# Performance work log

Measured on AMD Instinct MI355X. Metric: run time of the kernel, lower is better.

The kernel has to match this reference:

```python
import jax, jax.numpy as jnp
import numpy as np

B, S, D, A = 8, 4096, 128, 128


def _pos_encoding(seq_len, dim):
    # sin/cos positional encoding, same construction as the torch buffer
    pos = np.arange(seq_len, dtype=np.float32)[:, None]
    div = np.exp(np.arange(0, dim, 2, dtype=np.float32) * (-np.log(10000.0) / dim))
    pe = np.zeros((seq_len, dim), dtype=np.float32)
    pe[:, 0::2] = np.sin(pos * div)
    pe[:, 1::2] = np.cos(pos * div)
    return jnp.asarray(pe)


def setup_inputs() -> dict:
    key = jax.random.key(0)
    ks = jax.random.split(key, 7)
    sc = 1.0 / np.sqrt(D)
    return {
        "x": jax.random.normal(ks[0], (B, S, D), dtype=jnp.float32),
        "Wq": jax.random.normal(ks[1], (D, A), dtype=jnp.float32) * sc,
        "bq": jnp.zeros((A,), dtype=jnp.float32),
        "Wk": jax.random.normal(ks[2], (D, A), dtype=jnp.float32) * sc,
        "bk": jnp.zeros((A,), dtype=jnp.float32),
        "Wv": jax.random.normal(ks[3], (D, A), dtype=jnp.float32) * sc,
        "bv": jnp.zeros((A,), dtype=jnp.float32),
    }


def reference(x, Wq, bq, Wk, bk, Wv, bv):
    b, s, d = x.shape
    pe = _pos_encoding(s, d)  # [S, D]
    xp = x + pe[None]  # broadcast add of positional encoding
    q = xp @ Wq + bq  # [B, S, A]
    k = xp @ Wk + bk
    v = xp @ Wv + bv
    scale = 1.0 / jnp.sqrt(jnp.asarray(Wq.shape[1], dtype=jnp.float32))
    scores = jnp.einsum("bsa,bta->bst", q, k) * scale  # [B, S, S]
    weights = jax.nn.softmax(scores, axis=-1)
    out = jnp.einsum("bst,bta->bsa", weights, v)  # [B, S, A]
    return out
```

## Files before the change

### kernel.cpp

```cpp
#include <hip/hip_runtime.h>

#define BB 8
#define SS 4096
#define DD 128

typedef __attribute__((ext_vector_type(8))) short v8s;
typedef __attribute__((ext_vector_type(4))) float v4f;
typedef __attribute__((ext_vector_type(16))) float v16f;

__device__ __forceinline__ unsigned short f2bf(float f) {
    unsigned int u = __float_as_uint(f);
    u += 0x7fffu + ((u >> 16) & 1u);
    return (unsigned short)(u >> 16);
}
__device__ __forceinline__ unsigned int pk_bf16(float a, float b) {
    unsigned int ua = __float_as_uint(a) + 0x8000u;
    unsigned int ub = __float_as_uint(b) + 0x8000u;
    return __builtin_amdgcn_perm(ub, ua, 0x07060302u);
}

#if !defined(__HIP_DEVICE_COMPILE__)
#define MFMA16(a, b, c) (c)
#define MFMA32(a, b, c) (c)
#define GLDS16(g, l)
#define WAITVM(n)
#define WAITLGKM()
#define BAR()
#else
#define MFMA16(a, b, c) __builtin_amdgcn_mfma_f32_16x16x32_bf16((a), (b), (c), 0, 0, 0)
#define MFMA32(a, b, c) __builtin_amdgcn_mfma_f32_32x32x16_bf16((a), (b), (c), 0, 0, 0)
#define GLDS16(g, l)                                                         \
    __builtin_amdgcn_global_load_lds(                                        \
        (const __attribute__((address_space(1))) unsigned int*)(g),          \
        (__attribute__((address_space(3))) unsigned int*)(l), 16, 0, 0)
#define WAITVM(n) asm volatile("s_waitcnt vmcnt(" #n ")" ::: "memory")
#define WAITLGKM() asm volatile("s_waitcnt lgkmcnt(0)" ::: "memory")
#define BAR()                                                                \
    do {                                                                     \
        asm volatile("" ::: "memory");                                       \
        __builtin_amdgcn_s_barrier();                                        \
        __builtin_amdgcn_sched_barrier(0);                                   \
        asm volatile("" ::: "memory");                                       \
    } while (0)
#endif

#if !defined(__HIP_DEVICE_COMPILE__)
#define EXP2F(x) exp2f(x)
#elif __has_builtin(__builtin_amdgcn_exp2f)
#define EXP2F(x) __builtin_amdgcn_exp2f(x)
#else
#define EXP2F(x) exp2f(x)
#endif

#define QSCALE 0.12751743f

__global__ __launch_bounds__(256) void prep_kernel(
    const float* __restrict__ Wq, const float* __restrict__ Wk,
    const float* __restrict__ Wv, unsigned short* __restrict__ Wt,
    float* __restrict__ pe)
{
    int bid = blockIdx.x;
    int tid = threadIdx.x;
    if (bid < 192) {
        int id = bid * 256 + tid;
        int w = id >> 14;
        int n = (id >> 7) & 127;
        int k = id & 127;
        const float* W = (w == 0) ? Wq : (w == 1) ? Wk : Wv;
        Wt[id] = f2bf(W[k * 128 + n]);
    } else {
        int id = (bid - 192) * 256 + tid;
        int s = id >> 5;
        int d0 = (id & 31) * 4;
        v4f r;
#pragma unroll
        for (int j = 0; j < 4; j += 2) {
            float freq = __expf((float)(d0 + j) * -0.07195578415606394f);
            float arg = (float)s * freq;
            r[j] = __sinf(arg);
            r[j + 1] = __cosf(arg);
        }
        *(v4f*)(pe + (size_t)s * DD + d0) = r;
    }
}

__global__ __launch_bounds__(256, 3) void proj_kernel(
    const float* __restrict__ x, const float* __restrict__ pe,
    const unsigned short* __restrict__ Wt,
    const float* __restrict__ bq, const float* __restrict__ bk,
    const float* __restrict__ bv,
    unsigned short* __restrict__ qo, unsigned short* __restrict__ ko,
    unsigned short* __restrict__ vo)
{
    __shared__ __attribute__((aligned(16))) unsigned short w_lds[128 * 136];
    __shared__ __attribute__((aligned(16))) unsigned short o_lds[9216];

    const int tid = threadIdx.x;
    const int wave = tid >> 6;
    const int lane = tid & 63;
    const int quad = lane >> 4;
    const int l15 = lane & 15;
    const int bid = blockIdx.x;
    const int mat = bid % 3;
    const int rbase = (bid / 3) * 64;

    const unsigned short* Wp = Wt + (mat << 14);
#pragma unroll
    for (int it = 0; it < 8; ++it) {
        int id = it * 256 + tid;
        int n = id >> 4, c8 = id & 15;
        *(v8s*)(w_lds + n * 136 + c8 * 8) = *(const v8s*)(Wp + n * 128 + c8 * 8);
    }

    const int flatrow = rbase + wave * 16 + l15;
    const int srow = flatrow & 4095;
    v8s af[4];
#pragma unroll
    for (int kc = 0; kc < 4; ++kc) {
        const int kbase = kc * 32 + quad * 8;
        const v4f* xp = (const v4f*)(x + (size_t)flatrow * DD + kbase);
        const v4f* pp = (const v4f*)(pe + (size_t)srow * DD + kbase);
        v4f x0 = xp[0], x1 = xp[1], p0 = pp[0], p1 = pp[1];
        v8s a;
#pragma unroll
        for (int j = 0; j < 4; ++j) a[j] = (short)f2bf(x0[j] + p0[j]);
#pragma unroll
        for (int j = 0; j < 4; ++j) a[4 + j] = (short)f2bf(x1[j] + p1[j]);
        af[kc] = a;
    }

    const float* bias = (mat == 0) ? bq : (mat == 1) ? bk : bv;
    const int quadp = ((quad & 1) << 1) | (quad >> 1);
    __syncthreads();

#pragma unroll
    for (int nb = 0; nb < 8; ++nb) {
        const int col = nb * 16 + l15;
        v4f acc = {0.f, 0.f, 0.f, 0.f};
#pragma unroll
        for (int kc = 0; kc < 4; ++kc) {
            v8s bf = *(const v8s*)(w_lds + col * 136 + kc * 32 + quad * 8);
            acc = MFMA16(af[kc], bf, acc);
        }
        float bval = bias[col];
#pragma unroll
        for (int reg = 0; reg < 4; ++reg) {
            float val = acc[reg] + bval;
            if (mat == 0) {
                int lr = wave * 16 + quad * 4 + reg;
                o_lds[lr * 136 + col] = f2bf(val * QSCALE);
            } else if (mat == 1) {
                int lr = wave * 16 + quad * 4 + reg;
                o_lds[lr * 136 + col] = f2bf(val);
            } else {
                int plr = wave * 16 + quadp * 4 + reg;
                o_lds[col * 72 + plr] = f2bf(val);
            }
        }
    }
    __syncthreads();

    if (mat <= 1) {
        unsigned short* outp = (mat == 0) ? qo : ko;
#pragma unroll
        for (int it = 0; it < 4; ++it) {
            int id = it * 256 + tid;
            int r = id >> 4, c8 = id & 15;
            *(v8s*)(outp + (size_t)(rbase + r) * DD + c8 * 8) =
                *(const v8s*)(o_lds + r * 136 + c8 * 8);
        }
    } else {
        const int b0 = rbase >> 12, s0 = rbase & 4095;
#pragma unroll
        for (int it = 0; it < 4; ++it) {
            int id = it * 256 + tid;
            int a = id >> 3, c = id & 7;
            *(v8s*)(vo + ((size_t)(b0 * 128 + a)) * SS + s0 + c * 8) =
                *(const v8s*)(o_lds + a * 72 + c * 8);
        }
    }
}

#define KT 32
#define QKEYS 1024
#define NT2 (QKEYS / KT)
__global__ __launch_bounds__(512, 2) void flash_kernel(
    const unsigned short* __restrict__ qp,
    const unsigned short* __restrict__ kp,
    const unsigned short* __restrict__ vp,
    float* __restrict__ outp)
{
    __shared__ __attribute__((aligned(16))) unsigned short k_lds[4][2][4096];
    __shared__ __attribute__((aligned(16))) unsigned short v_lds[4][2][4096];
    __shared__ float xl[8][64];

    const int tid = threadIdx.x;
    const int wave = tid >> 6;
    const int lane = tid & 63;
    const int hi = lane >> 5;
    const int l31 = lane & 31;
    const int qtr = wave >> 1;
    const int w = wave & 1;
    const int qs = wave & 1;
    const int bid = blockIdx.x;
    const int b = bid & 7;
    const int qt = bid >> 3;
    const int qbase = qt * 128;

    const size_t qrow0 = (size_t)(b * SS + qbase + qs * 64 + l31) * DD;
    v8s qf0[8], qf1[8];
#pragma unroll
    for (int kc = 0; kc < 8; ++kc) {
        qf0[kc] = *(const v8s*)(qp + qrow0 + kc * 16 + hi * 8);
        qf1[kc] = *(const v8s*)(qp + qrow0 + (size_t)32 * DD + kc * 16 + hi * 8);
    }

    v16f o0[4], o1[4];
#pragma unroll
    for (int fg = 0; fg < 4; ++fg)
#pragma unroll
        for (int r = 0; r < 16; ++r) { o0[fg][r] = 0.f; o1[fg][r] = 0.f; }
    float lp0 = 0.f, lp1 = 0.f;

    const int koff = qtr * 16384 + l31 * 256 + ((hi << 4) ^ ((l31 & 7) << 4));
    const int hx3 = (hi << 4) ^ ((l31 & 3) << 4);
    const int vaddr0 = qtr * 16384 + l31 * 64 + hx3;
    const int vaddr1 = qtr * 16384 + l31 * 64 + (hx3 ^ 32);

    const int krw = lane >> 4, ksl = lane & 15;
    const int e_sh = krw * 128 + ((ksl ^ krw) << 3);
    const unsigned short* kq =
        kp + ((size_t)(b * SS) + qtr * QKEYS) * DD + w * 2048;
    const unsigned short* kp0_ = kq + e_sh;
    const unsigned short* kp4_ = kq + (e_sh ^ 32);
    const int vrw = lane >> 2, vsl = lane & 3;
    const int e_v = vrw * 4096 + ((vsl ^ (vrw & 3)) << 3);
    const unsigned short* vq =
        vp + (size_t)b * DD * SS + qtr * QKEYS + (size_t)w * 262144 + e_v;

    auto stage = [&](int p, int t) {
        unsigned short* kd = &k_lds[qtr][p][w * 2048];
        unsigned short* vd = &v_lds[qtr][p][w * 2048];
        const unsigned short* ks0 = kp0_ + (size_t)t * 4096;
        const unsigned short* ks4 = kp4_ + (size_t)t * 4096;
        const unsigned short* vs = vq + (size_t)t * 32;
        GLDS16(ks0, kd);
        GLDS16(ks4 + 512, kd + 512);
        GLDS16(ks0 + 1024, kd + 1024);
        GLDS16(ks4 + 1536, kd + 1536);
        GLDS16(vs, vd);
        GLDS16(vs + 65536, vd + 512);
        GLDS16(vs + 131072, vd + 1024);
        GLDS16(vs + 196608, vd + 1536);
    };

    auto compute = [&](int p) {
        v16f s0, s1;
#pragma unroll
        for (int r = 0; r < 16; ++r) { s0[r] = 0.f; s1[r] = 0.f; }
#pragma unroll
        for (int kc = 0; kc < 8; ++kc) {
            v8s af = *(const v8s*)((const char*)k_lds +
                                   ((koff ^ (kc << 5)) + p * 8192));
            s0 = MFMA32(af, qf0[kc], s0);
            s1 = MFMA32(af, qf1[kc], s1);
        }
        union PU { v8s v[2]; unsigned int u[8]; } P0, P1;
        float e[16];
#pragma unroll
        for (int r = 0; r < 16; ++r) e[r] = EXP2F(s0[r]);
        lp0 += (((e[0] + e[1]) + (e[2] + e[3])) + ((e[4] + e[5]) + (e[6] + e[7]))) +
               (((e[8] + e[9]) + (e[10] + e[11])) + ((e[12] + e[13]) + (e[14] + e[15])));
#pragma unroll
        for (int g = 0; g < 2; ++g)
#pragma unroll
            for (int m = 0; m < 4; ++m)
                P0.u[g * 4 + m] = pk_bf16(e[2 * m + 8 * g], e[2 * m + 8 * g + 1]);
#pragma unroll
        for (int r = 0; r < 16; ++r) e[r] = EXP2F(s1[r]);
        lp1 += (((e[0] + e[1]) + (e[2] + e[3])) + ((e[4] + e[5]) + (e[6] + e[7]))) +
               (((e[8] + e[9]) + (e[10] + e[11])) + ((e[12] + e[13]) + (e[14] + e[15])));
#pragma unroll
        for (int g = 0; g < 2; ++g)
#pragma unroll
            for (int m = 0; m < 4; ++m)
                P1.u[g * 4 + m] = pk_bf16(e[2 * m + 8 * g], e[2 * m + 8 * g + 1]);
#pragma unroll
        for (int g = 0; g < 2; ++g) {
            const int va = g ? vaddr1 : vaddr0;
#pragma unroll
            for (int fg = 0; fg < 4; ++fg) {
                v8s bf = *(const v8s*)((const char*)v_lds +
                                       (va + fg * 2048 + p * 8192));
                o0[fg] = MFMA32(P0.v[g], bf, o0[fg]);
                o1[fg] = MFMA32(P1.v[g], bf, o1[fg]);
            }
        }
    };

    stage(0, 0);
#pragma unroll 1
    for (int t = 0; t < NT2; t += 2) {
        stage(1, t + 1);
        WAITVM(8);
        BAR();
        compute(0);
        WAITLGKM();
        BAR();
        if (t + 2 < NT2) {
            stage(0, t + 2);
            WAITVM(8);
        } else {
            WAITVM(0);
        }
        BAR();
        compute(1);
        WAITLGKM();
        BAR();
    }

    lp0 += __shfl_xor(lp0, 32);
    lp1 += __shfl_xor(lp1, 32);
    if (hi == 0) { xl[wave][l31] = lp0; xl[wave][32 + l31] = lp1; }

    float* kf = (float*)&k_lds[0][0][0];
    float* vf = (float*)&v_lds[0][0][0];

    auto putO = [&](float* base) {
#pragma unroll
        for (int qgf = 0; qgf < 8; ++qgf) {
            const v16f& ov = (qgf < 4) ? o0[qgf] : o1[qgf - 4];
#pragma unroll
            for (int c = 0; c < 4; ++c) {
                v4f tv = {ov[c * 4 + 0], ov[c * 4 + 1], ov[c * 4 + 2], ov[c * 4 + 3]};
                *(v4f*)(base + (qgf * 4 + c) * 256 + lane * 4) = tv;
            }
        }
    };
    auto addO = [&](const float* base) {
#pragma unroll
        for (int qgf = 0; qgf < 8; ++qgf) {
            v16f& ov = (qgf < 4) ? o0[qgf] : o1[qgf - 4];
#pragma unroll
            for (int c = 0; c < 4; ++c) {
                v4f tv = *(const v4f*)(base + (qgf * 4 + c) * 256 + lane * 4);
#pragma unroll
                for (int j = 0; j < 4; ++j) ov[c * 4 + j] += tv[j];
            }
        }
    };

    if (qtr & 1) putO(((qtr == 1) ? kf : vf) + qs * 8192);
    __syncthreads();
    if (!(qtr & 1)) addO(((qtr == 0) ? kf : vf) + qs * 8192);
    __syncthreads();
    if (qtr == 2) putO(kf + qs * 8192);
    __syncthreads();
    if (qtr == 0) {
        addO(kf + qs * 8192);
#pragma unroll
        for (int qg2 = 0; qg2 < 2; ++qg2) {
            float ir[16];
#pragma unroll
            for (int r = 0; r < 16; ++r) {
                int qrow = (r & 3) + 8 * (r >> 2) + 4 * hi;
                float ls = xl[0 + qs][qg2 * 32 + qrow] + xl[2 + qs][qg2 * 32 + qrow] +
                           xl[4 + qs][qg2 * 32 + qrow] + xl[6 + qs][qg2 * 32 + qrow];
                ir[r] = 1.0f / ls;
            }
#pragma unroll
            for (int fg = 0; fg < 4; ++fg) {
                const v16f& ov = qg2 ? o1[fg] : o0[fg];
#pragma unroll
                for (int r = 0; r < 16; ++r) {
                    int qrow = (r & 3) + 8 * (r >> 2) + 4 * hi;
                    outp[(size_t)(b * SS + qbase + qs * 64 + qg2 * 32 + qrow) * DD +
                         fg * 32 + l31] = ov[r] * ir[r];
                }
            }
        }
    }
}

extern "C" void kernel_launch(void* const* d_in, const int* in_sizes, int n_in,
                              void* d_out, int out_size, void* d_ws, size_t ws_size,
                              hipStream_t stream)
{
    const float* x  = (const float*)d_in[0];
    const float* Wq = (const float*)d_in[1];
    const float* bq = (const float*)d_in[2];
    const float* Wk = (const float*)d_in[3];
    const float* bk = (const float*)d_in[4];
    const float* Wv = (const float*)d_in[5];
    const float* bv = (const float*)d_in[6];
    float* out = (float*)d_out;

    unsigned short* Wt = (unsigned short*)d_ws;
    unsigned short* q  = Wt + 49152;
    unsigned short* k  = q + (size_t)BB * SS * DD;
    unsigned short* vT = k + (size_t)BB * SS * DD;
    float* pe = (float*)(vT + (size_t)BB * SS * DD);

    hipLaunchKernelGGL(prep_kernel, dim3(704), dim3(256), 0, stream,
                       Wq, Wk, Wv, Wt, pe);
    hipLaunchKernelGGL(proj_kernel, dim3(BB * SS / 64 * 3), dim3(256), 0, stream,
                       x, pe, Wt, bq, bk, bv, q, k, vT);
    hipLaunchKernelGGL(flash_kernel, dim3(BB * SS / 128), dim3(512), 0, stream,
                       q, k, vT, out);
}
```

Before: 202.4 us.

## Split keys in halves, load K fragments directly to registers, simplify merge

The flash kernel's work split changes from four key quarters times two 64-row query groups to two key halves times four 32-row query groups. Each wave now loads its K fragments straight from global memory into registers, double-buffered, so only V is staged through LDS. The cross-wave merge shrinks to a single put/add step through a dedicated LDS buffer with a lane-swizzled layout. This cuts LDS traffic, K staging and merge barriers. In exchange, each wave reuses each K tile for only 32 query rows, so K is read more from global/L2, and the extra K registers may raise register pressure.

```diff
diff --git a/kernel.cpp b/kernel.cpp
--- a/kernel.cpp
+++ b/kernel.cpp
@@ -182,203 +182,170 @@
 }
 
 #define KT 32
-#define QKEYS 1024
-#define NT2 (QKEYS / KT)
+#define HKEYS 2048
+#define NT (HKEYS / KT)
 __global__ __launch_bounds__(512, 2) void flash_kernel(
     const unsigned short* __restrict__ qp,
     const unsigned short* __restrict__ kp,
     const unsigned short* __restrict__ vp,
     float* __restrict__ outp)
 {
-    __shared__ __attribute__((aligned(16))) unsigned short k_lds[4][2][4096];
-    __shared__ __attribute__((aligned(16))) unsigned short v_lds[4][2][4096];
-    __shared__ float xl[8][64];
+    __shared__ __attribute__((aligned(16))) unsigned short v_lds[2][2][4096];
+    __shared__ __attribute__((aligned(16))) float merge_lds[16384];
+    __shared__ float xl[8][32];
 
     const int tid = threadIdx.x;
     const int wave = tid >> 6;
     const int lane = tid & 63;
     const int hi = lane >> 5;
     const int l31 = lane & 31;
-    const int qtr = wave >> 1;
-    const int w = wave & 1;
-    const int qs = wave & 1;
+    const int half = wave >> 2;
+    const int qs = wave & 3;
+    const int wv = wave & 3;
     const int bid = blockIdx.x;
     const int b = bid & 7;
     const int qt = bid >> 3;
     const int qbase = qt * 128;
 
-    const size_t qrow0 = (size_t)(b * SS + qbase + qs * 64 + l31) * DD;
-    v8s qf0[8], qf1[8];
-#pragma unroll
-    for (int kc = 0; kc < 8; ++kc) {
-        qf0[kc] = *(const v8s*)(qp + qrow0 + kc * 16 + hi * 8);
-        qf1[kc] = *(const v8s*)(qp + qrow0 + (size_t)32 * DD + kc * 16 + hi * 8);
-    }
-
-    v16f o0[4], o1[4];
+    const size_t qrow = (size_t)(b * SS + qbase + qs * 32 + l31) * DD;
+    v8s qf[8];
+#pragma unroll
+    for (int kc = 0; kc < 8; ++kc)
+        qf[kc] = *(const v8s*)(qp + qrow + kc * 16 + hi * 8);
+
+    v16f o[4];
 #pragma unroll
     for (int fg = 0; fg < 4; ++fg)
 #pragma unroll
-        for (int r = 0; r < 16; ++r) { o0[fg][r] = 0.f; o1[fg][r] = 0.f; }
-    float lp0 = 0.f, lp1 = 0.f;
-
-    const int koff = qtr * 16384 + l31 * 256 + ((hi << 4) ^ ((l31 & 7) << 4));
+        for (int r = 0; r < 16; ++r) o[fg][r] = 0.f;
+    float lp = 0.f;
+
+    const unsigned short* kbase =
+        kp + ((size_t)(b * SS + half * HKEYS + l31)) * DD + hi * 8;
+
     const int hx3 = (hi << 4) ^ ((l31 & 3) << 4);
-    const int vaddr0 = qtr * 16384 + l31 * 64 + hx3;
-    const int vaddr1 = qtr * 16384 + l31 * 64 + (hx3 ^ 32);
-
-    const int krw = lane >> 4, ksl = lane & 15;
-    const int e_sh = krw * 128 + ((ksl ^ krw) << 3);
-    const unsigned short* kq =
-        kp + ((size_t)(b * SS) + qtr * QKEYS) * DD + w * 2048;
-    const unsigned short* kp0_ = kq + e_sh;
-    const unsigned short* kp4_ = kq + (e_sh ^ 32);
+    const int va0 = half * 16384 + l31 * 64 + hx3;
+    const int va1 = va0 ^ 32;
+
     const int vrw = lane >> 2, vsl = lane & 3;
-    const int e_v = vrw * 4096 + ((vsl ^ (vrw & 3)) << 3);
-    const unsigned short* vq =
-        vp + (size_t)b * DD * SS + qtr * QKEYS + (size_t)w * 262144 + e_v;
-
-    auto stage = [&](int p, int t) {
-        unsigned short* kd = &k_lds[qtr][p][w * 2048];
-        unsigned short* vd = &v_lds[qtr][p][w * 2048];
-        const unsigned short* ks0 = kp0_ + (size_t)t * 4096;
-        const unsigned short* ks4 = kp4_ + (size_t)t * 4096;
-        const unsigned short* vs = vq + (size_t)t * 32;
-        GLDS16(ks0, kd);
-        GLDS16(ks4 + 512, kd + 512);
-        GLDS16(ks0 + 1024, kd + 1024);
-        GLDS16(ks4 + 1536, kd + 1536);
+    const unsigned short* vsrc =
+        vp + (size_t)b * DD * SS + (size_t)(wv * 32 + vrw) * SS +
+        half * HKEYS + ((vsl ^ (vrw & 3)) << 3);
+
+    auto stageV = [&](int p, int t) {
+        unsigned short* vd = &v_lds[half][p][wv * 1024];
+        const unsigned short* vs = vsrc + t * KT;
         GLDS16(vs, vd);
-        GLDS16(vs + 65536, vd + 512);
-        GLDS16(vs + 131072, vd + 1024);
-        GLDS16(vs + 196608, vd + 1536);
-    };
-
-    auto compute = [&](int p) {
-        v16f s0, s1;
-#pragma unroll
-        for (int r = 0; r < 16; ++r) { s0[r] = 0.f; s1[r] = 0.f; }
-#pragma unroll
-        for (int kc = 0; kc < 8; ++kc) {
-            v8s af = *(const v8s*)((const char*)k_lds +
-                                   ((koff ^ (kc << 5)) + p * 8192));
-            s0 = MFMA32(af, qf0[kc], s0);
-            s1 = MFMA32(af, qf1[kc], s1);
-        }
-        union PU { v8s v[2]; unsigned int u[8]; } P0, P1;
+        GLDS16(vs + (size_t)16 * SS, vd + 512);
+    };
+    auto loadK = [&](v8s (&kf)[8], int t) {
+        const unsigned short* kr = kbase + (size_t)t * KT * DD;
+#pragma unroll
+        for (int kc = 0; kc < 8; ++kc)
+            kf[kc] = *(const v8s*)(kr + kc * 16);
+    };
+    auto compute = [&](int p, const v8s (&kf)[8]) {
+        v16f s;
+#pragma unroll
+        for (int r = 0; r < 16; ++r) s[r] = 0.f;
+#pragma unroll
+        for (int kc = 0; kc < 8; ++kc)
+            s = MFMA32(kf[kc], qf[kc], s);
         float e[16];
 #pragma unroll
-        for (int r = 0; r < 16; ++r) e[r] = EXP2F(s0[r]);
-        lp0 += (((e[0] + e[1]) + (e[2] + e[3])) + ((e[4] + e[5]) + (e[6] + e[7]))) +
-               (((e[8] + e[9]) + (e[10] + e[11])) + ((e[12] + e[13]) + (e[14] + e[15])));
+        for (int r = 0; r < 16; ++r) e[r] = EXP2F(s[r]);
+        lp += (((e[0] + e[1]) + (e[2] + e[3])) + ((e[4] + e[5]) + (e[6] + e[7]))) +
+              (((e[8] + e[9]) + (e[10] + e[11])) + ((e[12] + e[13]) + (e[14] + e[15])));
+        union { v8s v[2]; unsigned int u[8]; } P;
 #pragma unroll
         for (int g = 0; g < 2; ++g)
 #pragma unroll
             for (int m = 0; m < 4; ++m)
-                P0.u[g * 4 + m] = pk_bf16(e[2 * m + 8 * g], e[2 * m + 8 * g + 1]);
-#pragma unroll
-        for (int r = 0; r < 16; ++r) e[r] = EXP2F(s1[r]);
-        lp1 += (((e[0] + e[1]) + (e[2] + e[3])) + ((e[4] + e[5]) + (e[6] + e[7]))) +
-               (((e[8] + e[9]) + (e[10] + e[11])) + ((e[12] + e[13]) + (e[14] + e[15])));
-#pragma unroll
-        for (int g = 0; g < 2; ++g)
-#pragma unroll
-            for (int m = 0; m < 4; ++m)
-                P1.u[g * 4 + m] = pk_bf16(e[2 * m + 8 * g], e[2 * m + 8 * g + 1]);
+                P.u[g * 4 + m] = pk_bf16(e[2 * m + 8 * g], e[2 * m + 8 * g + 1]);
 #pragma unroll
         for (int g = 0; g < 2; ++g) {
-            const int va = g ? vaddr1 : vaddr0;
+            const int va = g ? va1 : va0;
 #pragma unroll
             for (int fg = 0; fg < 4; ++fg) {
                 v8s bf = *(const v8s*)((const char*)v_lds +
-                                       (va + fg * 2048 + p * 8192));
-                o0[fg] = MFMA32(P0.v[g], bf, o0[fg]);
-                o1[fg] = MFMA32(P1.v[g], bf, o1[fg]);
-            }
-        }
-    };
-
-    stage(0, 0);
+                                       (va + p * 8192 + fg * 2048));
+                o[fg] = MFMA32(P.v[g], bf, o[fg]);
+            }
+        }
+    };
+
+    v8s kfA[8], kfB[8];
+
+    stageV(0, 0);
+    loadK(kfA, 0);
 #pragma unroll 1
-    for (int t = 0; t < NT2; t += 2) {
-        stage(1, t + 1);
-        WAITVM(8);
+    for (int t = 0; t < NT; t += 2) {
+        stageV(1, t + 1);
+        loadK(kfB, t + 1);
+        WAITVM(10);
         BAR();
-        compute(0);
+        compute(0, kfA);
         WAITLGKM();
         BAR();
-        if (t + 2 < NT2) {
-            stage(0, t + 2);
-            WAITVM(8);
+        if (t + 2 < NT) {
+            stageV(0, t + 2);
+            loadK(kfA, t + 2);
+            WAITVM(10);
         } else {
             WAITVM(0);
         }
         BAR();
-        compute(1);
+        compute(1, kfB);
         WAITLGKM();
         BAR();
     }
 
-    lp0 += __shfl_xor(lp0, 32);
-    lp1 += __shfl_xor(lp1, 32);
-    if (hi == 0) { xl[wave][l31] = lp0; xl[wave][32 + l31] = lp1; }
-
-    float* kf = (float*)&k_lds[0][0][0];
-    float* vf = (float*)&v_lds[0][0][0];
+    lp += __shfl_xor(lp, 32);
+    if (hi == 0) xl[wave][l31] = lp;
 
     auto putO = [&](float* base) {
 #pragma unroll
-        for (int qgf = 0; qgf < 8; ++qgf) {
-            const v16f& ov = (qgf < 4) ? o0[qgf] : o1[qgf - 4];
+        for (int fg = 0; fg < 4; ++fg) {
+            float* bp = base + fg * 1024 + lane * 16;
 #pragma unroll
             for (int c = 0; c < 4; ++c) {
-                v4f tv = {ov[c * 4 + 0], ov[c * 4 + 1], ov[c * 4 + 2], ov[c * 4 + 3]};
-                *(v4f*)(base + (qgf * 4 + c) * 256 + lane * 4) = tv;
+                v4f tv = {o[fg][c * 4 + 0], o[fg][c * 4 + 1],
+                          o[fg][c * 4 + 2], o[fg][c * 4 + 3]};
+                ((v4f*)bp)[c ^ (lane & 3)] = tv;
             }
         }
     };
     auto addO = [&](const float* base) {
 #pragma unroll
-        for (int qgf = 0; qgf < 8; ++qgf) {
-            v16f& ov = (qgf < 4) ? o0[qgf] : o1[qgf - 4];
+        for (int fg = 0; fg < 4; ++fg) {
+            const float* bp = base + fg * 1024 + lane * 16;
 #pragma unroll
             for (int c = 0; c < 4; ++c) {
-                v4f tv = *(const v4f*)(base + (qgf * 4 + c) * 256 + lane * 4);
-#pragma unroll
-                for (int j = 0; j < 4; ++j) ov[c * 4 + j] += tv[j];
-            }
-        }
-    };
-
-    if (qtr & 1) putO(((qtr == 1) ? kf : vf) + qs * 8192);
+                v4f tv = ((const v4f*)bp)[c ^ (lane & 3)];
+#pragma unroll
+                for (int j = 0; j < 4; ++j) o[fg][c * 4 + j] += tv[j];
+            }
+        }
+    };
+
+    if (half == 1) putO(merge_lds + qs * 4096);
     __syncthreads();
-    if (!(qtr & 1)) addO(((qtr == 0) ? kf : vf) + qs * 8192);
-    __syncthreads();
-    if (qtr == 2) putO(kf + qs * 8192);
-    __syncthreads();
-    if (qtr == 0) {
-        addO(kf + qs * 8192);
-#pragma unroll
-        for (int qg2 = 0; qg2 < 2; ++qg2) {
-            float ir[16];
+    if (half == 0) {
+        addO(merge_lds + qs * 4096);
+        float ir[16];
+#pragma unroll
+        for (int r = 0; r < 16; ++r) {
+            int qr = (r & 3) + 8 * (r >> 2) + 4 * hi;
+            ir[r] = 1.0f / (xl[qs][qr] + xl[4 + qs][qr]);
+        }
+#pragma unroll
+        for (int fg = 0; fg < 4; ++fg)
 #pragma unroll
             for (int r = 0; r < 16; ++r) {
-                int qrow = (r & 3) + 8 * (r >> 2) + 4 * hi;
-                float ls = xl[0 + qs][qg2 * 32 + qrow] + xl[2 + qs][qg2 * 32 + qrow] +
-                           xl[4 + qs][qg2 * 32 + qrow] + xl[6 + qs][qg2 * 32 + qrow];
-                ir[r] = 1.0f / ls;
-            }
-#pragma unroll
-            for (int fg = 0; fg < 4; ++fg) {
-                const v16f& ov = qg2 ? o1[fg] : o0[fg];
-#pragma unroll
-                for (int r = 0; r < 16; ++r) {
-                    int qrow = (r & 3) + 8 * (r >> 2) + 4 * hi;
-                    outp[(size_t)(b * SS + qbase + qs * 64 + qg2 * 32 + qrow) * DD +
-                         fg * 32 + l31] = ov[r] * ir[r];
-                }
-            }
-        }
+                int qr = (r & 3) + 8 * (r >> 2) + 4 * hi;
+                outp[(size_t)(b * SS + qbase + qs * 32 + qr) * DD +
+                     fg * 32 + l31] = o[fg][r] * ir[r];
+            }
     }
 }
 
```

Result: slower. 270.5 us (+33.6%).
